# Kernel tuning notes

Measured on AMD Instinct MI355X. Metric: run time of the kernel, lower is better.

Reference implementation:

```python
import jax, jax.numpy as jnp
import numpy as np

NUM_HEADS = 8
WINDOW = 64
ENCODERS = 6
EPS = 1e-5


def _positional_encoding(S, D, dtype=jnp.float32):
    pos = jnp.arange(S, dtype=jnp.float32)[:, None]
    div = jnp.exp(-jnp.log(10000.0) * jnp.arange(0, D, 2, dtype=jnp.float32) / D)
    ang = pos * div  # [S, D/2]
    pe = jnp.zeros((S, D), dtype=jnp.float32)
    pe = pe.at[:, 0::2].set(jnp.sin(ang)).at[:, 1::2].set(jnp.cos(ang))
    return pe.astype(dtype)


def _layernorm(x, g, b):
    mu = jnp.mean(x, axis=-1, keepdims=True)
    var = jnp.var(x, axis=-1, keepdims=True)
    return (x - mu) * jax.lax.rsqrt(var + EPS) * g + b


def _local_attention(x, wq, bq, wk, bk, wv, bv, window_mask):
    B, S, D = x.shape
    Dh = D // NUM_HEADS
    scale = Dh ** -0.5
    def split(t):  # [B,S,D] -> [B,H,S,Dh]
        return t.reshape(B, S, NUM_HEADS, Dh).transpose(0, 2, 1, 3)
    q = split(x @ wq.T + bq)
    k = split(x @ wk.T + bk)
    v = split(x @ wv.T + bv)
    scores = jnp.einsum('bhqd,bhkd->bhqk', q, k)
    # FAITHFUL: out-of-window entries are ZERO (not -inf); softmax over full S.
    scores = jnp.where(window_mask, scores, 0.0) * scale
    probs = jax.nn.softmax(scores, axis=-1)
    out = jnp.einsum('bhqk,bhkd->bhqd', probs, v)
    return out.transpose(0, 2, 1, 3).reshape(B, S, D)


def reference(inputs, emb, wq, bq, wk, bk, wv, bv, ln_g, ln_b,
              fc1_w, fc1_b, fc2_w, fc2_b, out_w, out_b):
    B, S = inputs.shape
    D = emb.shape[1]
    # window slice in torch source: [max(0, i-W), min(S, i+W))  (end exclusive)
    i = jnp.arange(S)[:, None]
    j = jnp.arange(S)[None, :]
    window_mask = (j >= i - WINDOW) & (j < i + WINDOW)  # [S, S]

    x = emb[inputs]  # [B, S, D]
    x = x + _positional_encoding(S, D, x.dtype)
    for _ in range(ENCODERS):  # shared weights across encoder iterations
        a = _local_attention(x, wq, bq, wk, bk, wv, bv, window_mask)
        x = _layernorm(a, ln_g, ln_b)
        h = jax.nn.relu(x @ fc1_w.T + fc1_b)
        x = (h @ fc2_w.T + fc2_b) + x
        x = _layernorm(x, ln_g, ln_b)
    x = x.reshape(B, S * D)
    return x @ out_w.T + out_b


def setup_inputs() -> dict:
    key = jax.random.key(0)
    ks = jax.random.split(key, 16)
    B, S, D, Hd, V, C = 8, 1024, 512, 2048, 32000, 6
    s = 0.02
    return {
        'inputs': jax.random.randint(ks[0], (B, S), 0, 31999),
        'emb': jax.random.normal(ks[1], (V, D), jnp.float32) * s,
        'wq': jax.random.normal(ks[2], (D, D), jnp.float32) * s,
        'bq': jnp.zeros((D,), jnp.float32),
        'wk': jax.random.normal(ks[3], (D, D), jnp.float32) * s,
        'bk': jnp.zeros((D,), jnp.float32),
        'wv': jax.random.normal(ks[4], (D, D), jnp.float32) * s,
        'bv': jnp.zeros((D,), jnp.float32),
        'ln_g': jnp.ones((D,), jnp.float32),
        'ln_b': jnp.zeros((D,), jnp.float32),
        'fc1_w': jax.random.normal(ks[5], (Hd, D), jnp.float32) * s,
        'fc1_b': jnp.zeros((Hd,), jnp.float32),
        'fc2_w': jax.random.normal(ks[6], (D, Hd), jnp.float32) * s,
        'fc2_b': jnp.zeros((D,), jnp.float32),
        'out_w': jax.random.normal(ks[7], (C, S * D), jnp.float32) * s,
        'out_b': jnp.zeros((C,), jnp.float32),
    }
```

## Files before the change

### kernel.cpp

```cpp
#include <hip/hip_runtime.h>

#define S_LEN 1024
#define DMODEL 512
#define NHEADS 8
#define DHEAD 64
#define HDIM 2048
#define WIN 64

typedef _Float16 f16x8 __attribute__((ext_vector_type(8)));
typedef _Float16 f16x2 __attribute__((ext_vector_type(2)));
typedef float f32x4 __attribute__((ext_vector_type(4)));
typedef float f32x16 __attribute__((ext_vector_type(16)));

__device__ __forceinline__ void stage16(const _Float16* g, _Float16* l) {
  __builtin_amdgcn_global_load_lds((const __attribute__((address_space(1))) unsigned int*)g,
                                   (__attribute__((address_space(3))) unsigned int*)l, 16, 0, 0);
}

__global__ void wprep_kernel(const float* __restrict__ wq, const float* __restrict__ wk,
                             const float* __restrict__ wv, const float* __restrict__ bq,
                             const float* __restrict__ bk, const float* __restrict__ bv,
                             const float* __restrict__ w1, const float* __restrict__ w2,
                             const float* __restrict__ wo,
                             _Float16* __restrict__ Wqkv, float* __restrict__ bqkv,
                             _Float16* __restrict__ W1h, _Float16* __restrict__ W2h,
                             _Float16* __restrict__ Woh) {
  int i = blockIdx.x * 256 + threadIdx.x;
  if (i < 262144) {
    Wqkv[i]          = (_Float16)wq[i];
    Wqkv[262144 + i] = (_Float16)wk[i];
    Wqkv[524288 + i] = (_Float16)wv[i];
  }
  if (i < 1048576) {
    W1h[i] = (_Float16)w1[i];
    W2h[i] = (_Float16)w2[i];
    Woh[i]           = (_Float16)wo[i];
    Woh[1048576 + i] = (_Float16)wo[1048576 + i];
    Woh[2097152 + i] = (_Float16)wo[2097152 + i];
  }
  if (i < 512) { bqkv[i] = bq[i]; bqkv[512 + i] = bk[i]; bqkv[1024 + i] = bv[i]; }
}

__global__ void embed_pe_kernel(const int* __restrict__ inputs, const float* __restrict__ emb,
                                _Float16* __restrict__ Xb) {
  int row = blockIdx.x;
  int s = row & (S_LEN - 1);
  int t = threadIdx.x;
  int tok = inputs[row];
  float dv = __expf(-logf(10000.0f) * (2.0f * (float)t) / (float)DMODEL);
  float ang = (float)s * dv;
  float sv = sinf(ang);
  float cv = cosf(ang);
  size_t base = (size_t)row * DMODEL + 2 * t;
  float x0 = emb[(size_t)tok * DMODEL + 2 * t] + sv;
  float x1 = emb[(size_t)tok * DMODEL + 2 * t + 1] + cv;
  f16x2 h; h[0] = (_Float16)x0; h[1] = (_Float16)x1;
  *(f16x2*)(Xb + base) = h;
}

#define EPI_RELU16 1
#define EPI_QKV 3
#define EPI_PART 4

template <int EPI>
__launch_bounds__(256)
__global__ void mfma_gemm(const _Float16* __restrict__ A, const _Float16* __restrict__ W,
                          const float* __restrict__ bias,
                          float* __restrict__ Cf0, float* __restrict__ Cf1,
                          _Float16* __restrict__ Ch, float* __restrict__ VS,
                          int M, int N, int Kstride, int Kslice) {
  __shared__ _Float16 As[128 * 32];
  __shared__ _Float16 Bs[128 * 32];
  const int bm = blockIdx.x * 128;
  const int bn = blockIdx.y * 128;
  const int z = blockIdx.z;
  const int t = threadIdx.x;
  const int lane = t & 63;
  const int w = t >> 6;
  const int wr = w >> 1, wc = w & 1;
  const int l15 = lane & 15, l4 = lane >> 4;

  const int idx0 = t, idx1 = t + 256;
  const int r0 = idx0 >> 2, kg0 = (idx0 & 3) << 3;
  const int r1 = idx1 >> 2, kg1 = (idx1 & 3) << 3;
  const _Float16* Ag0 = A + (size_t)(bm + r0) * Kstride + kg0;
  const _Float16* Ag1 = A + (size_t)(bm + r1) * Kstride + kg1;
  const _Float16* Wg0 = W + (size_t)(bn + r0) * Kstride + kg0;
  const _Float16* Wg1 = W + (size_t)(bn + r1) * Kstride + kg1;
  _Float16* Al0 = As + idx0 * 8;
  _Float16* Al1 = As + idx1 * 8;
  _Float16* Bl0 = Bs + idx0 * 8;
  _Float16* Bl1 = Bs + idx1 * 8;

  const int kbeg = z * Kslice, kend = kbeg + Kslice;
  f32x4 acc[4][4] = {};
  for (int k0 = kbeg; k0 < kend; k0 += 32) {
    stage16(Ag0 + k0, Al0);
    stage16(Ag1 + k0, Al1);
    stage16(Wg0 + k0, Bl0);
    stage16(Wg1 + k0, Bl1);
    __syncthreads();
    f16x8 af[4], bf[4];
#pragma unroll
    for (int m = 0; m < 4; ++m)
      af[m] = *(const f16x8*)&As[(wr * 64 + m * 16 + l15) * 32 + l4 * 8];
#pragma unroll
    for (int n = 0; n < 4; ++n)
      bf[n] = *(const f16x8*)&Bs[(wc * 64 + n * 16 + l15) * 32 + l4 * 8];
#pragma unroll
    for (int m = 0; m < 4; ++m)
#pragma unroll
      for (int n = 0; n < 4; ++n)
        acc[m][n] = __builtin_amdgcn_mfma_f32_16x16x32_f16(af[m], bf[n], acc[m][n], 0, 0, 0);
    __syncthreads();
  }
  float* dst = (EPI == EPI_PART) ? (z ? Cf1 : Cf0) : Cf0;
  float cs[4] = {0.f, 0.f, 0.f, 0.f};
#pragma unroll
  for (int n = 0; n < 4; ++n) {
    int col = bn + wc * 64 + n * 16 + l15;
    float bb = (EPI == EPI_PART) ? 0.f : bias[col];
#pragma unroll
    for (int m = 0; m < 4; ++m) {
      int row = bm + wr * 64 + m * 16 + l4 * 4;
#pragma unroll
      for (int j = 0; j < 4; ++j) {
        float v = acc[m][n][j] + bb;
        if (EPI == EPI_RELU16) {
          v = fmaxf(v, 0.0f);
          Ch[(size_t)(row + j) * N + col] = (_Float16)v;
        } else if (EPI == EPI_QKV) {
          Ch[(size_t)(row + j) * N + col] = (_Float16)v;
          cs[n] += v;
        } else {
          dst[(size_t)(row + j) * N + col] = v;
        }
      }
    }
  }
  if (EPI == EPI_QKV && bn >= 1024) {
    const int batch = bm >> 10;
#pragma unroll
    for (int n = 0; n < 4; ++n) {
      float s = cs[n];
      s += __shfl_xor(s, 16);
      s += __shfl_xor(s, 32);
      if (l4 == 0) {
        int col = bn + wc * 64 + n * 16 + l15;
        atomicAdd(&VS[batch * 512 + (col - 1024)], s);
      }
    }
  }
}

__global__ void vs_zero_kernel(float* __restrict__ VS) {
  VS[blockIdx.x * 256 + threadIdx.x] = 0.0f;
}

#define KTMAX 256
#define VTS 264

__launch_bounds__(256)
__global__ void attn_kernel(const _Float16* __restrict__ QKVh, const float* __restrict__ VSg,
                            float* __restrict__ O) {
  __shared__ _Float16 Ks[KTMAX * 64];
  __shared__ _Float16 Vt[64 * VTS];
  __shared__ float VsC[8][64];

  const int qb0 = blockIdx.x * 128, h = blockIdx.y, b = blockIdx.z;
  const int jlo = max(0, qb0 - WIN);
  const int jhi = min(S_LEN, qb0 + 128 + WIN);
  const int KT = jhi - jlo;
  const int t = threadIdx.x;
  const int lane = t & 63, w = t >> 6;
  const int hi = lane >> 5, l31 = lane & 31;

  const _Float16* Kg = QKVh + ((size_t)(b * S_LEN + jlo)) * 1536 + 512 + h * 64;
#pragma unroll
  for (int p = 0; p < 8; ++p) {
    int u = t + p * 256;
    int row = u >> 3;
    int cb = (u & 7) * 16;
    int rowc = min(row, KT - 1);
    int scb = cb ^ ((row & 7) << 4);
    stage16(Kg + (size_t)rowc * 1536 + (scb >> 1), Ks + u * 8);
  }
  const _Float16* Vg = QKVh + ((size_t)(b * S_LEN + jlo)) * 1536 + 1024 + h * 64;
#pragma unroll
  for (int p = 0; p < 8; ++p) {
    int u = t + p * 256;
    int row = u >> 3;
    int d0 = (u & 7) * 8;
    f16x8 v = {0, 0, 0, 0, 0, 0, 0, 0};
    if (row < KT) v = *(const f16x8*)(Vg + (size_t)row * 1536 + d0);
#pragma unroll
    for (int e = 0; e < 8; ++e) Vt[(d0 + e) * VTS + row] = v[e];
  }
  __syncthreads();
  for (int slot = t; slot < 512; slot += 256) {
    int c = slot >> 6, d = slot & 63;
    const f16x8* col = (const f16x8*)(Vt + d * VTS + c * 32);
    float s = 0.f;
#pragma unroll
    for (int g = 0; g < 4; ++g) {
      f16x8 v = col[g];
#pragma unroll
      for (int e = 0; e < 8; ++e) s += (float)v[e];
    }
    VsC[c][d] = s;
  }
  const int qw = qb0 + w * 32;
  const _Float16* Qg = QKVh + ((size_t)(b * S_LEN + qw + l31)) * 1536 + h * 64;
  f16x8 qf[4];
#pragma unroll
  for (int ds = 0; ds < 4; ++ds) qf[ds] = *(const f16x8*)(Qg + ds * 16 + hi * 8);
  __syncthreads();

  const int c0 = max(0, qw - WIN - jlo) >> 5;
  const int c1 = min(KT, qw + 96 - jlo) >> 5;
  const int nproc = (c1 - c0) * 32;
  const int i = qw + l31;
  const int wlo = i - WIN, whi = i + WIN;

  float m = 0.f, l = 0.f;
  f32x16 accA = {}, accB = {};

  union PK { f16x2 h; unsigned u; };
  union A8 { unsigned u[4]; f16x8 h; };

  for (int c = c0; c < c1; ++c) {
    const int kb = c * 32;
    f32x16 sf = {};
#pragma unroll
    for (int ds = 0; ds < 4; ++ds) {
      int row = kb + l31;
      int cbyte = ((ds * 16 + hi * 8) * 2) ^ ((row & 7) << 4);
      f16x8 kf = *(const f16x8*)((const char*)Ks + row * 128 + cbyte);
      sf = __builtin_amdgcn_mfma_f32_32x32x16_f16(kf, qf[ds], sf, 0, 0, 0);
    }
    float s[16]; float pm = -1e30f;
#pragma unroll
    for (int r = 0; r < 16; ++r) {
      int gk = jlo + kb + (r & 3) + 8 * (r >> 2) + 4 * hi;
      float v = (gk >= wlo && gk < whi) ? sf[r] * 0.125f : 0.f;
      s[r] = v;
      pm = fmaxf(pm, v);
    }
    pm = fmaxf(pm, __shfl_xor(pm, 32));
    if (!__all(pm <= m + 8.f)) {
      float mn = fmaxf(m, pm);
      float f = __expf(m - mn);
      l *= f;
#pragma unroll
      for (int r = 0; r < 16; ++r) {
        int q = (r & 3) + 8 * (r >> 2) + 4 * hi;
        float fr = __shfl(f, q);
        accA[r] *= fr; accB[r] *= fr;
      }
      m = mn;
    }
    float p[16]; float ls = 0.f;
#pragma unroll
    for (int r = 0; r < 16; ++r) { p[r] = __expf(s[r] - m); ls += p[r]; }
    l += ls;
    unsigned u[8], x[8];
#pragma unroll
    for (int kk = 0; kk < 8; ++kk) {
      PK cv; cv.h[0] = (_Float16)p[2 * kk]; cv.h[1] = (_Float16)p[2 * kk + 1];
      u[kk] = cv.u;
    }
#pragma unroll
    for (int kk = 0; kk < 8; ++kk) x[kk] = (unsigned)__shfl_xor((int)u[kk], 32);
    A8 a0, a1;
    a0.u[0] = hi ? x[2] : u[0]; a0.u[1] = hi ? x[3] : u[1];
    a0.u[2] = hi ? u[2] : x[0]; a0.u[3] = hi ? u[3] : x[1];
    a1.u[0] = hi ? x[6] : u[4]; a1.u[1] = hi ? x[7] : u[5];
    a1.u[2] = hi ? u[6] : x[4]; a1.u[3] = hi ? u[7] : x[5];
#pragma unroll
    for (int ks = 0; ks < 2; ++ks) {
      f16x8 pa = ks ? a1.h : a0.h;
      f16x8 v0 = *(const f16x8*)(Vt + (size_t)(l31) * VTS + kb + ks * 16 + hi * 8);
      f16x8 v1 = *(const f16x8*)(Vt + (size_t)(32 + l31) * VTS + kb + ks * 16 + hi * 8);
      accA = __builtin_amdgcn_mfma_f32_32x32x16_f16(pa, v0, accA, 0, 0, 0);
      accB = __builtin_amdgcn_mfma_f32_32x32x16_f16(pa, v1, accB, 0, 0, 0);
    }
  }

  l = l + __shfl_xor(l, 32);
  const int dA = l31, dB = 32 + l31;
  float vsA = 0.f, vsB = 0.f;
  for (int c = c0; c < c1; ++c) { vsA += VsC[c][dA]; vsB += VsC[c][dB]; }
  const float vtA = VSg[b * 512 + h * 64 + dA];
  const float vtB = VSg[b * 512 + h * 64 + dB];
  const float zcount = (float)(S_LEN - nproc);
#pragma unroll
  for (int r = 0; r < 16; ++r) {
    int q = (r & 3) + 8 * (r >> 2) + 4 * hi;
    float mq = __shfl(m, q);
    float lq = __shfl(l, q);
    float em = __expf(-mq);
    float denom = lq + zcount * em;
    float inv = 1.0f / denom;
    size_t rowbase = ((size_t)(b * S_LEN + qw + q)) * DMODEL + h * 64;
    O[rowbase + dA] = (accA[r] + em * (vtA - vsA)) * inv;
    O[rowbase + dB] = (accB[r] + em * (vtB - vsB)) * inv;
  }
}

__global__ void ln_kernel(const float* __restrict__ X, const float* __restrict__ g,
                          const float* __restrict__ be, float* __restrict__ Y,
                          _Float16* __restrict__ Yh) {
  int row = blockIdx.x;
  int t = threadIdx.x;
  const float* x = X + (size_t)row * DMODEL;
  float2 v = *(const float2*)(x + 2 * t);
  float s = v.x + v.y;
  float sq = v.x * v.x + v.y * v.y;
#pragma unroll
  for (int off = 32; off; off >>= 1) {
    s += __shfl_xor(s, off);
    sq += __shfl_xor(sq, off);
  }
  __shared__ float ss[4], sqq[4];
  int w = t >> 6, lane = t & 63;
  if (lane == 0) { ss[w] = s; sqq[w] = sq; }
  __syncthreads();
  s = ss[0] + ss[1] + ss[2] + ss[3];
  sq = sqq[0] + sqq[1] + sqq[2] + sqq[3];
  float mu = s * (1.0f / DMODEL);
  float var = sq * (1.0f / DMODEL) - mu * mu;
  float rstd = rsqrtf(var + 1e-5f);
  float g0 = g[2 * t], g1 = g[2 * t + 1];
  float b0 = be[2 * t], b1 = be[2 * t + 1];
  float2 o;
  o.x = (v.x - mu) * rstd * g0 + b0;
  o.y = (v.y - mu) * rstd * g1 + b1;
  *(float2*)(Y + (size_t)row * DMODEL + 2 * t) = o;
  f16x2 hh; hh[0] = (_Float16)o.x; hh[1] = (_Float16)o.y;
  *(f16x2*)(Yh + (size_t)row * DMODEL + 2 * t) = hh;
}

__global__ void ln2_fused_kernel(const float* __restrict__ P0, const float* __restrict__ P1,
                                 const float* __restrict__ XB, const float* __restrict__ fb,
                                 const float* __restrict__ g, const float* __restrict__ be,
                                 _Float16* __restrict__ Yh) {
  int row = blockIdx.x;
  int t = threadIdx.x;
  size_t off = (size_t)row * DMODEL + 2 * t;
  float2 p0 = *(const float2*)(P0 + off);
  float2 p1 = *(const float2*)(P1 + off);
  float2 xb = *(const float2*)(XB + off);
  float2 v;
  v.x = p0.x + p1.x + fb[2 * t]     + xb.x;
  v.y = p0.y + p1.y + fb[2 * t + 1] + xb.y;
  float s = v.x + v.y;
  float sq = v.x * v.x + v.y * v.y;
#pragma unroll
  for (int off2 = 32; off2; off2 >>= 1) {
    s += __shfl_xor(s, off2);
    sq += __shfl_xor(sq, off2);
  }
  __shared__ float ss[4], sqq[4];
  int w = t >> 6, lane = t & 63;
  if (lane == 0) { ss[w] = s; sqq[w] = sq; }
  __syncthreads();
  s = ss[0] + ss[1] + ss[2] + ss[3];
  sq = sqq[0] + sqq[1] + sqq[2] + sqq[3];
  float mu = s * (1.0f / DMODEL);
  float var = sq * (1.0f / DMODEL) - mu * mu;
  float rstd = rsqrtf(var + 1e-5f);
  float g0 = g[2 * t], g1 = g[2 * t + 1];
  float b0 = be[2 * t], b1 = be[2 * t + 1];
  f16x2 hh;
  hh[0] = (_Float16)((v.x - mu) * rstd * g0 + b0);
  hh[1] = (_Float16)((v.y - mu) * rstd * g1 + b1);
  *(f16x2*)(Yh + off) = hh;
}

__global__ void outproj_partial_kernel(const _Float16* __restrict__ Xb,
                                       const _Float16* __restrict__ Woh,
                                       float* __restrict__ part) {
  const int KTOT = S_LEN * DMODEL;
  const int CH = KTOT / 16;
  int chunk = blockIdx.x, b = blockIdx.y;
  const int t = threadIdx.x;
  const _Float16* x = Xb + (size_t)b * KTOT + (size_t)chunk * CH;
  f16x8 xa[16];
#pragma unroll
  for (int p = 0; p < 16; ++p) xa[p] = *(const f16x8*)(x + (p * 256 + t) * 8);
  __shared__ float red[6][4];
  for (int c = 0; c < 6; ++c) {
    const _Float16* wv = Woh + (size_t)c * KTOT + (size_t)chunk * CH;
    float acc = 0.f;
#pragma unroll
    for (int p = 0; p < 16; ++p) {
      f16x8 wa = *(const f16x8*)(wv + (p * 256 + t) * 8);
#pragma unroll
      for (int e = 0; e < 8; ++e) acc += (float)xa[p][e] * (float)wa[e];
    }
#pragma unroll
    for (int off = 32; off; off >>= 1) acc += __shfl_xor(acc, off);
    if ((t & 63) == 0) red[c][t >> 6] = acc;
  }
  __syncthreads();
  if (t < 6)
    part[(b * 6 + t) * 16 + chunk] = red[t][0] + red[t][1] + red[t][2] + red[t][3];
}

__global__ void outproj_final_kernel(const float* __restrict__ part, const float* __restrict__ ob,
                                     float* __restrict__ out) {
  int idx = threadIdx.x;
  if (idx < 48) {
    float s = 0.f;
#pragma unroll
    for (int k = 0; k < 16; ++k) s += part[idx * 16 + k];
    out[idx] = s + ob[idx % 6];
  }
}

extern "C" void kernel_launch(void* const* d_in, const int* in_sizes, int n_in,
                              void* d_out, int out_size, void* d_ws, size_t ws_size,
                              hipStream_t stream) {
  (void)in_sizes; (void)n_in; (void)out_size; (void)ws_size;
  const int*   inputs = (const int*)  d_in[0];
  const float* emb    = (const float*)d_in[1];
  const float* wq     = (const float*)d_in[2];
  const float* bq     = (const float*)d_in[3];
  const float* wk     = (const float*)d_in[4];
  const float* bk     = (const float*)d_in[5];
  const float* wv     = (const float*)d_in[6];
  const float* bv     = (const float*)d_in[7];
  const float* ln_g   = (const float*)d_in[8];
  const float* ln_b   = (const float*)d_in[9];
  const float* fc1_w  = (const float*)d_in[10];
  const float* fc1_b  = (const float*)d_in[11];
  const float* fc2_w  = (const float*)d_in[12];
  const float* fc2_b  = (const float*)d_in[13];
  const float* out_w  = (const float*)d_in[14];
  const float* out_b  = (const float*)d_in[15];
  float* out = (float*)d_out;

  const int M = 8192;
  char* p = (char*)d_ws;
  float*    P0   = (float*)p;      p += (size_t)M * 512 * 4;
  _Float16* Xb   = (_Float16*)p;   p += (size_t)M * 512 * 2;
  _Float16* QKVh = (_Float16*)p;   p += (size_t)M * 1536 * 2;
  float*    XB   = (float*)p;      p += (size_t)M * 512 * 4;
  _Float16* XBb  = (_Float16*)p;   p += (size_t)M * 512 * 2;
  _Float16* H    = (_Float16*)p;   p += (size_t)M * 2048 * 2;
  float*    Ab   = (float*)H;
  _Float16* Wqkv = (_Float16*)p;   p += (size_t)1536 * 512 * 2;
  _Float16* W1h  = (_Float16*)p;   p += (size_t)2048 * 512 * 2;
  _Float16* W2h  = (_Float16*)p;   p += (size_t)512 * 2048 * 2;
  _Float16* Woh  = (_Float16*)p;   p += (size_t)6 * 524288 * 2;
  float*    bqkv = (float*)p;      p += 1536 * 4;
  float*    VS   = (float*)p;      p += 4096 * 4;
  float*    part = (float*)p;      p += 768 * 4;
  float*    P1   = (float*)QKVh;

  wprep_kernel<<<4096, 256, 0, stream>>>(wq, wk, wv, bq, bk, bv, fc1_w, fc2_w, out_w,
                                         Wqkv, bqkv, W1h, W2h, Woh);
  embed_pe_kernel<<<8192, 256, 0, stream>>>(inputs, emb, Xb);
  for (int it = 0; it < 6; ++it) {
    vs_zero_kernel<<<16, 256, 0, stream>>>(VS);
    mfma_gemm<EPI_QKV><<<dim3(64, 12), 256, 0, stream>>>(Xb, Wqkv, bqkv, nullptr, nullptr,
                                                         QKVh, VS, M, 1536, 512, 512);
    attn_kernel<<<dim3(8, 8, 8), 256, 0, stream>>>(QKVh, VS, Ab);
    ln_kernel<<<8192, 256, 0, stream>>>(Ab, ln_g, ln_b, XB, XBb);
    mfma_gemm<EPI_RELU16><<<dim3(64, 16), 256, 0, stream>>>(XBb, W1h, fc1_b, nullptr, nullptr,
                                                            H, nullptr, M, 2048, 512, 512);
    mfma_gemm<EPI_PART><<<dim3(64, 4, 2), 256, 0, stream>>>(H, W2h, nullptr, P0, P1,
                                                            nullptr, nullptr, M, 512, 2048, 1024);
    ln2_fused_kernel<<<8192, 256, 0, stream>>>(P0, P1, XB, fc2_b, ln_g, ln_b, Xb);
  }
  outproj_partial_kernel<<<dim3(16, 8), 256, 0, stream>>>(Xb, Woh, part);
  outproj_final_kernel<<<1, 64, 0, stream>>>(part, out_b, out);
}
```

Baseline: 856.5 us.

## Double-buffer GEMM LDS staging and widen out-projection grid

The MFMA GEMM now uses two LDS buffers. The global_load_lds for the next K-step is issued before computing the current one, so there is one barrier per step and the load latency overlaps the MFMA work. Separately, the out-projection partial kernel is split across classes and twice as many chunks, going from 128 blocks to 1536, which gives more parallelism. The cost is double the LDS per block, which may reduce occupancy, plus extra x re-reads per class. One concern: the async LDS loads may not be waited on before the barrier, which could create a correctness or timing risk.

Result: faster. 782.9 us (-8.6%).

```diff
diff --git a/kernel.cpp b/kernel.cpp
--- a/kernel.cpp
+++ b/kernel.cpp
@@ -69,8 +69,8 @@
                           float* __restrict__ Cf0, float* __restrict__ Cf1,
                           _Float16* __restrict__ Ch, float* __restrict__ VS,
                           int M, int N, int Kstride, int Kslice) {
-  __shared__ _Float16 As[128 * 32];
-  __shared__ _Float16 Bs[128 * 32];
+  __shared__ _Float16 As[2][128 * 32];
+  __shared__ _Float16 Bs[2][128 * 32];
   const int bm = blockIdx.x * 128;
   const int bn = blockIdx.y * 128;
   const int z = blockIdx.z;
@@ -87,33 +87,42 @@
   const _Float16* Ag1 = A + (size_t)(bm + r1) * Kstride + kg1;
   const _Float16* Wg0 = W + (size_t)(bn + r0) * Kstride + kg0;
   const _Float16* Wg1 = W + (size_t)(bn + r1) * Kstride + kg1;
-  _Float16* Al0 = As + idx0 * 8;
-  _Float16* Al1 = As + idx1 * 8;
-  _Float16* Bl0 = Bs + idx0 * 8;
-  _Float16* Bl1 = Bs + idx1 * 8;
-
-  const int kbeg = z * Kslice, kend = kbeg + Kslice;
+
+  const int kbeg = z * Kslice;
+  const int nsteps = Kslice >> 5;
+
+  stage16(Ag0 + kbeg, As[0] + idx0 * 8);
+  stage16(Ag1 + kbeg, As[0] + idx1 * 8);
+  stage16(Wg0 + kbeg, Bs[0] + idx0 * 8);
+  stage16(Wg1 + kbeg, Bs[0] + idx1 * 8);
+  __syncthreads();
+
   f32x4 acc[4][4] = {};
-  for (int k0 = kbeg; k0 < kend; k0 += 32) {
-    stage16(Ag0 + k0, Al0);
-    stage16(Ag1 + k0, Al1);
-    stage16(Wg0 + k0, Bl0);
-    stage16(Wg1 + k0, Bl1);
-    __syncthreads();
+  int cur = 0;
+  for (int s = 0; s < nsteps; ++s) {
+    if (s + 1 < nsteps) {
+      int kn = kbeg + (s + 1) * 32;
+      stage16(Ag0 + kn, As[cur ^ 1] + idx0 * 8);
+      stage16(Ag1 + kn, As[cur ^ 1] + idx1 * 8);
+      stage16(Wg0 + kn, Bs[cur ^ 1] + idx0 * 8);
+      stage16(Wg1 + kn, Bs[cur ^ 1] + idx1 * 8);
+    }
     f16x8 af[4], bf[4];
 #pragma unroll
     for (int m = 0; m < 4; ++m)
-      af[m] = *(const f16x8*)&As[(wr * 64 + m * 16 + l15) * 32 + l4 * 8];
+      af[m] = *(const f16x8*)&As[cur][(wr * 64 + m * 16 + l15) * 32 + l4 * 8];
 #pragma unroll
     for (int n = 0; n < 4; ++n)
-      bf[n] = *(const f16x8*)&Bs[(wc * 64 + n * 16 + l15) * 32 + l4 * 8];
+      bf[n] = *(const f16x8*)&Bs[cur][(wc * 64 + n * 16 + l15) * 32 + l4 * 8];
 #pragma unroll
     for (int m = 0; m < 4; ++m)
 #pragma unroll
       for (int n = 0; n < 4; ++n)
         acc[m][n] = __builtin_amdgcn_mfma_f32_16x16x32_f16(af[m], bf[n], acc[m][n], 0, 0, 0);
     __syncthreads();
-  }
+    cur ^= 1;
+  }
+
   float* dst = (EPI == EPI_PART) ? (z ? Cf1 : Cf0) : Cf0;
   float cs[4] = {0.f, 0.f, 0.f, 0.f};
 #pragma unroll
@@ -381,30 +390,27 @@
                                        const _Float16* __restrict__ Woh,
                                        float* __restrict__ part) {
   const int KTOT = S_LEN * DMODEL;
-  const int CH = KTOT / 16;
-  int chunk = blockIdx.x, b = blockIdx.y;
+  const int CH = KTOT / 32;
+  int chunk = blockIdx.x, c = blockIdx.y, b = blockIdx.z;
   const int t = threadIdx.x;
   const _Float16* x = Xb + (size_t)b * KTOT + (size_t)chunk * CH;
-  f16x8 xa[16];
-#pragma unroll
-  for (int p = 0; p < 16; ++p) xa[p] = *(const f16x8*)(x + (p * 256 + t) * 8);
-  __shared__ float red[6][4];
-  for (int c = 0; c < 6; ++c) {
-    const _Float16* wv = Woh + (size_t)c * KTOT + (size_t)chunk * CH;
-    float acc = 0.f;
-#pragma unroll
-    for (int p = 0; p < 16; ++p) {
-      f16x8 wa = *(const f16x8*)(wv + (p * 256 + t) * 8);
-#pragma unroll
-      for (int e = 0; e < 8; ++e) acc += (float)xa[p][e] * (float)wa[e];
-    }
-#pragma unroll
-    for (int off = 32; off; off >>= 1) acc += __shfl_xor(acc, off);
-    if ((t & 63) == 0) red[c][t >> 6] = acc;
-  }
-  __syncthreads();
-  if (t < 6)
-    part[(b * 6 + t) * 16 + chunk] = red[t][0] + red[t][1] + red[t][2] + red[t][3];
+  const _Float16* wv = Woh + (size_t)c * KTOT + (size_t)chunk * CH;
+  float acc = 0.f;
+#pragma unroll
+  for (int p = 0; p < 8; ++p) {
+    f16x8 a = *(const f16x8*)(x + (p * 256 + t) * 8);
+    f16x8 w8 = *(const f16x8*)(wv + (p * 256 + t) * 8);
+#pragma unroll
+    for (int e = 0; e < 8; ++e) acc += (float)a[e] * (float)w8[e];
+  }
+#pragma unroll
+  for (int off = 32; off; off >>= 1) acc += __shfl_xor(acc, off);
+  __shared__ float red[4];
+  int w = t >> 6, lane = t & 63;
+  if (lane == 0) red[w] = acc;
+  __syncthreads();
+  if (t == 0)
+    part[(b * 6 + c) * 32 + chunk] = red[0] + red[1] + red[2] + red[3];
 }
 
 __global__ void outproj_final_kernel(const float* __restrict__ part, const float* __restrict__ ob,
@@ -413,7 +419,7 @@
   if (idx < 48) {
     float s = 0.f;
 #pragma unroll
-    for (int k = 0; k < 16; ++k) s += part[idx * 16 + k];
+    for (int k = 0; k < 32; ++k) s += part[idx * 32 + k];
     out[idx] = s + ob[idx % 6];
   }
 }
@@ -455,7 +461,7 @@
   _Float16* Woh  = (_Float16*)p;   p += (size_t)6 * 524288 * 2;
   float*    bqkv = (float*)p;      p += 1536 * 4;
   float*    VS   = (float*)p;      p += 4096 * 4;
-  float*    part = (float*)p;      p += 768 * 4;
+  float*    part = (float*)p;      p += 1536 * 4;
   float*    P1   = (float*)QKVh;
 
   wprep_kernel<<<4096, 256, 0, stream>>>(wq, wk, wv, bq, bk, bv, fc1_w, fc2_w, out_w,
@@ -473,6 +479,6 @@
                                                             nullptr, nullptr, M, 512, 2048, 1024);
     ln2_fused_kernel<<<8192, 256, 0, stream>>>(P0, P1, XB, fc2_b, ln_g, ln_b, Xb);
   }
-  outproj_partial_kernel<<<dim3(16, 8), 256, 0, stream>>>(Xb, Woh, part);
+  outproj_partial_kernel<<<dim3(32, 6, 8), 256, 0, stream>>>(Xb, Woh, part);
   outproj_final_kernel<<<1, 64, 0, stream>>>(part, out_b, out);
 }
```
